# Kernel tuning notes

Hardware: AMD Instinct MI355X
Metric: run time of the kernel (lower is better)

Reference implementation:

```python
import jax, jax.numpy as jnp
import numpy as np

K = 3
STRIDE = 1
PAD = 1
DIL = 1


def setup_inputs() -> dict:
    key = jax.random.key(0)
    k1, k2, k3 = jax.random.split(key, 3)
    B, C, O, H, W = 8, 64, 64, 128, 128
    x = jax.random.normal(k1, (B, C, H, W), dtype=jnp.float32)
    # small offset-conv weights so predicted offsets stay in a sane range
    w_off = jax.random.normal(k2, (2 * K * K, C, K, K), dtype=jnp.float32) * 0.05
    b_off = jnp.zeros((2 * K * K,), dtype=jnp.float32)
    w_conv = jax.random.normal(k3, (O, C, K, K), dtype=jnp.float32) * (1.0 / np.sqrt(C * K * K))
    return {"x": x, "w_off": w_off, "b_off": b_off, "w_conv": w_conv}


def _offset_conv(x, w, b):
    y = jax.lax.conv_general_dilated(
        x, w, window_strides=(STRIDE, STRIDE),
        padding=[(PAD, PAD), (PAD, PAD)], rhs_dilation=(DIL, DIL),
        dimension_numbers=("NCHW", "OIHW", "NCHW"))
    return y + b[None, :, None, None]


def _deform_conv2d(x, offset, weight):
    # torchvision deform_conv2d v1, groups=1, offset_groups=1, no bias
    B, C, H, W = x.shape
    Ho, Wo = offset.shape[2], offset.shape[3]
    # offset channels laid out as (ky, kx, [dy, dx]) pairs
    off = offset.reshape(B, K, K, 2, Ho, Wo)
    dy, dx = off[:, :, :, 0], off[:, :, :, 1]           # [B,K,K,Ho,Wo]

    hs = (jnp.arange(Ho) * STRIDE - PAD).astype(offset.dtype)
    ws = (jnp.arange(Wo) * STRIDE - PAD).astype(offset.dtype)
    kk = (jnp.arange(K) * DIL).astype(offset.dtype)
    py = hs[None, None, None, :, None] + kk[None, :, None, None, None] + dy
    px = ws[None, None, None, None, :] + kk[None, None, :, None, None] + dx

    y0 = jnp.floor(py)
    x0 = jnp.floor(px)
    ly = py - y0
    lx = px - x0
    y0i = y0.astype(jnp.int32)
    x0i = x0.astype(jnp.int32)

    xf = x.reshape(B, C, H * W)

    def gather(yi, xi):
        valid = ((yi >= 0) & (yi < H) & (xi >= 0) & (xi < W)).astype(x.dtype)
        idx = jnp.clip(yi, 0, H - 1) * W + jnp.clip(xi, 0, W - 1)  # [B,K,K,Ho,Wo]
        idxf = idx.reshape(B, 1, -1)
        v = jnp.take_along_axis(xf, idxf, axis=2)                  # [B,C,K*K*Ho*Wo]
        v = v.reshape(B, C, K, K, Ho, Wo)
        return v * valid[:, None]                                  # zero-pad out of bounds

    ly_ = ly[:, None]  # broadcast over channel dim
    lx_ = lx[:, None]
    val = (gather(y0i, x0i) * (1 - ly_) * (1 - lx_)
           + gather(y0i, x0i + 1) * (1 - ly_) * lx_
           + gather(y0i + 1, x0i) * ly_ * (1 - lx_)
           + gather(y0i + 1, x0i + 1) * ly_ * lx_)   # [B,C,K,K,Ho,Wo]

    return jnp.einsum("bcklhw,ockl->bohw", val, weight)


def reference(x, w_off, b_off, w_conv):
    offset = _offset_conv(x, w_off, b_off)
    return _deform_conv2d(x, offset, w_conv)
```

## Files before the change

### kernel.cpp

```cpp
#include <hip/hip_runtime.h>

#define B_    8
#define C_    64
#define O_    64
#define H_    128
#define W_    128
#define HW_   (H_ * W_)
#define NOFF_ 18
#define KK_   9
#define TW_   19
#define PADW_ 5
#define RSTR_ 144

typedef __attribute__((ext_vector_type(8))) _Float16 f16x8;
typedef __attribute__((ext_vector_type(2))) _Float16 f16x2;
typedef __attribute__((ext_vector_type(4))) unsigned int u32x4;
typedef __attribute__((ext_vector_type(4))) float f32x4;
typedef unsigned int uint32;
typedef unsigned short ushort;

__device__ __forceinline__ f16x2 u2h(uint32 u) {
    union { uint32 u; f16x2 h; } c; c.u = u; return c.h;
}
__device__ __forceinline__ f16x8 u2h8(u32x4 q) {
    union { u32x4 u; f16x8 h; } c; c.u = q; return c.h;
}

#define GLOAD16(dst, a64) \
    asm volatile("global_load_dwordx4 %0, %1, off" : "=&v"(dst) : "v"(a64) : "memory")
#define WAITV_TIE(N, w) \
    asm volatile("s_waitcnt vmcnt(" #N ")" \
        : "+v"(w[0]), "+v"(w[1]), "+v"(w[2]), "+v"(w[3]), \
          "+v"(w[4]), "+v"(w[5]), "+v"(w[6]), "+v"(w[7]))
#define WAITV(N) do { \
    asm volatile("s_waitcnt vmcnt(" #N ")" ::: "memory"); \
    __builtin_amdgcn_sched_barrier(0); } while (0)
#define DRAIN_ALL() do { \
    asm volatile("s_waitcnt vmcnt(0) lgkmcnt(0)" ::: "memory"); \
    __builtin_amdgcn_sched_barrier(0); } while (0)

__global__ __launch_bounds__(256) void transpose_x(
    const float* __restrict__ x, _Float16* __restrict__ xT)
{
    __shared__ float tile[64][65];
    int blk = blockIdx.x;
    int b   = blk >> 8;
    int hw0 = (blk & 255) * 64;
    int t   = threadIdx.x;
    int q   = t >> 6;
    int ln  = t & 63;
#pragma unroll
    for (int p = 0; p < 16; ++p) {
        int c = p * 4 + q;
        tile[c][ln] = x[((size_t)(b * C_ + c) << 14) + hw0 + ln];
    }
    __syncthreads();
#pragma unroll
    for (int p = 0; p < 16; ++p) {
        int hw = p * 4 + q;
        xT[(((size_t)b << 14) + hw0 + hw) * 64 + ln] = (_Float16)tile[ln][hw];
    }
}

__global__ __launch_bounds__(256) void prep3(
    const float* __restrict__ w_conv, const float* __restrict__ w_off,
    _Float16* __restrict__ wfrag, _Float16* __restrict__ wofff)
{
    int idx = blockIdx.x * 256 + threadIdx.x;
    if (idx < 36864) {
        int i    = idx & 7;
        int lane = (idx >> 3) & 63;
        int nb   = (idx >> 9) & 3;
        int kc   = (idx >> 11) & 1;
        int kk   = idx >> 12;
        int c = kc * 32 + ((lane >> 4) << 3) + i;
        int o = nb * 16 + (lane & 15);
        wfrag[idx] = (_Float16)w_conv[(o * C_ + c) * 9 + kk];
    }
    if (idx < 18432) {
        int i    = idx & 7;
        int lane = (idx >> 3) & 63;
        int nb   = (idx >> 9) & 1;
        int kc   = (idx >> 10) & 1;
        int kk   = idx >> 11;
        int m = nb * 16 + (lane & 15);
        int c = kc * 32 + ((lane >> 4) << 3) + i;
        wofff[idx] = (_Float16)((m < NOFF_) ? w_off[(m * C_ + c) * 9 + kk] : 0.0f);
    }
}

__global__ __launch_bounds__(512, 2) void offconv_mfma5(
    const _Float16* __restrict__ xT, const _Float16* __restrict__ wofff,
    const float* __restrict__ b_off, _Float16* __restrict__ offsh)
{
    __shared__ _Float16 wlds[18432];
    int t = threadIdx.x;
    {
        const u32x4* src = (const u32x4*)wofff;
        u32x4* dst = (u32x4*)wlds;
#pragma unroll
        for (int r = 0; r < 5; ++r) {
            int i = r * 512 + t;
            if (i < 2304) dst[i] = src[i];
        }
    }
    DRAIN_ALL();
    __syncthreads();

    int blk  = blockIdx.x;
    int b    = blk & 7;
    int hw0  = (blk >> 3) * 128;
    int lane = t & 63;
    int wv   = t >> 6;
    int pxb  = hw0 + wv * 16;
    int pr   = lane & 15;
    int g    = lane >> 4;
    int px   = pxb + pr;
    int h = px >> 7, w = px & (W_ - 1);
    const _Float16* xb = xT + (((size_t)b << 14) << 6);

    f32x4 acc[2];
#pragma unroll
    for (int nb = 0; nb < 2; ++nb) acc[nb] = (f32x4){0.f, 0.f, 0.f, 0.f};

    u32x4 q[3][2];
    bool  vld[3];

    auto issueO = [&](int kk, int st) {
        int ky = kk / 3, kx = kk % 3;
        int yy = h - 1 + ky, xx = w - 1 + kx;
        vld[st] = ((unsigned)yy < (unsigned)H_) && ((unsigned)xx < (unsigned)W_);
        int src = (min(max(yy, 0), H_ - 1) << 7) + min(max(xx, 0), W_ - 1);
        unsigned long long a = (unsigned long long)(xb + ((size_t)src << 6) + g * 8);
        GLOAD16(q[st][0], a);
        unsigned long long a2 = a + 64;
        GLOAD16(q[st][1], a2);
    };

    issueO(0, 0); issueO(1, 1); issueO(2, 2);
#pragma unroll
    for (int kk = 0; kk < KK_; ++kk) {
        const int s = kk % 3;
        if (kk < 7)      { WAITV(4); }
        else if (kk < 8) { WAITV(2); }
        else             { WAITV(0); }
#pragma unroll
        for (int kc = 0; kc < 2; ++kc) {
            f16x8 a = u2h8(q[s][kc]);
            f16x8 z = {};
            a = vld[s] ? a : z;
#pragma unroll
            for (int nb = 0; nb < 2; ++nb) {
                f16x8 bfr = *(const f16x8*)(wlds +
                    ((((kk * 2 + kc) << 1) + nb) << 9) + (lane << 3));
                acc[nb] = __builtin_amdgcn_mfma_f32_16x16x32_f16(a, bfr, acc[nb], 0, 0, 0);
            }
        }
        if (kk < 6) issueO(kk + 3, s);
    }

#pragma unroll
    for (int nb = 0; nb < 2; ++nb) {
        int m = nb * 16 + pr;
        if (m < NOFF_) {
            float bias = b_off[m];
#pragma unroll
            for (int r = 0; r < 4; ++r) {
                int prow = pxb + g * 4 + r;
                offsh[(size_t)((b << 14) + prow) * NOFF_ + m] = (_Float16)(acc[nb][r] + bias);
            }
        }
    }
}

__global__ __launch_bounds__(256, 3) void deform_mfma10(
    const _Float16* __restrict__ xT, const _Float16* __restrict__ offsh,
    const _Float16* __restrict__ wfrag, float* __restrict__ out)
{
    __shared__ char tilec[TW_ * TW_ * RSTR_];

    int t    = threadIdx.x;
    int blk  = blockIdx.x;
    int b    = blk & 7;
    int tid  = blk >> 3;
    int ty   = tid >> 4, tx = tid & 15;
    int lane = t & 63;
    int wv   = t >> 6;
    int pr   = lane & 15;
    int gg   = lane >> 4;
    int ry0  = ty * 8 - PADW_;
    int cx0  = tx * 8 - PADW_;
    const _Float16* xb = xT + (((size_t)b << 14) << 6);

#pragma unroll
    for (int it = 0; it < 12; ++it) {
        int idx = it * 256 + t;
        if (idx < TW_ * TW_ * 8) {
            int i   = idx / (TW_ * 8);
            int rem = idx - i * (TW_ * 8);
            int j   = rem >> 3, cg = rem & 7;
            int yy = min(max(ry0 + i, 0), H_ - 1);
            int xx = min(max(cx0 + j, 0), W_ - 1);
            u32x4 v = *(const u32x4*)(xb + (((size_t)((yy << 7) + xx)) << 6) + (cg << 3));
            int rl = i * TW_ + j;
            *(u32x4*)(tilec + rl * RSTR_ + (cg << 4)) = v;
        }
    }

    int h_img = ty * 8 + wv * 2 + (pr >> 3);
    int w_img = tx * 8 + (pr & 7);
    const uint32* obu = (const uint32*)(offsh +
        (size_t)((b << 14) + (h_img << 7) + w_img) * NOFF_);
    uint32 dpk[9];
#pragma unroll
    for (int kk = 0; kk < 9; ++kk) dpk[kk] = obu[kk];
    DRAIN_ALL();
    __syncthreads();

    f32x4 acc[4];
#pragma unroll
    for (int nb = 0; nb < 4; ++nb) acc[nb] = (f32x4){0.f, 0.f, 0.f, 0.f};

    u32x4 wqA[8], wqB[8];
    u32x4 q[8];

    auto issueW = [&](int kk, u32x4* wq) {
#pragma unroll
        for (int f = 0; f < 8; ++f) {
            unsigned long long wa = (unsigned long long)(wfrag +
                ((((kk * 2 + (f >> 2)) << 2) + (f & 3)) << 9) + (lane << 3));
            GLOAD16(wq[f], wa);
        }
    };

    issueW(0, wqA);
#pragma unroll
    for (int kk = 0; kk < KK_; ++kk) {
        u32x4* wcur = (kk & 1) ? wqB : wqA;
        u32x4* wnxt = (kk & 1) ? wqA : wqB;
        if (kk < 8) issueW(kk + 1, wnxt);

        int ky = kk / 3, kx = kk % 3;
        union { uint32 u; f16x2 hh; } cv; cv.u = dpk[kk];
        float dyv = (float)cv.hh[0], dxv = (float)cv.hh[1];
        float py  = (float)(h_img - 1 + ky) + dyv;
        float pxf = (float)(w_img - 1 + kx) + dxv;
        float y0f = floorf(py), x0f = floorf(pxf);
        float ly = py - y0f, lx = pxf - x0f;
        int y0 = (int)y0f, x0 = (int)x0f;
        float w00 = (1.f - ly) * (1.f - lx);
        float w01 = (1.f - ly) * lx;
        float w10 = ly * (1.f - lx);
        float w11 = ly * lx;
        bool vy0 = (unsigned)y0       < (unsigned)H_;
        bool vy1 = (unsigned)(y0 + 1) < (unsigned)H_;
        bool vx0 = (unsigned)x0       < (unsigned)W_;
        bool vx1 = (unsigned)(x0 + 1) < (unsigned)W_;
        if (!(vy0 && vx0)) w00 = 0.f;
        if (!(vy0 && vx1)) w01 = 0.f;
        if (!(vy1 && vx0)) w10 = 0.f;
        if (!(vy1 && vx1)) w11 = 0.f;
        int yc0 = min(max(y0, 0), H_ - 1);
        int yc1 = min(max(y0 + 1, 0), H_ - 1);
        int xc0 = min(max(x0, 0), W_ - 1);
        int xc1 = min(max(x0 + 1, 0), W_ - 1);
        f16x2 Wc0 = (f16x2){(_Float16)w00, (_Float16)w00};
        f16x2 Wc1 = (f16x2){(_Float16)w01, (_Float16)w01};
        f16x2 Wc2 = (f16x2){(_Float16)w10, (_Float16)w10};
        f16x2 Wc3 = (f16x2){(_Float16)w11, (_Float16)w11};

        int r0 = yc0 - ry0, r1 = yc1 - ry0;
        int c0 = xc0 - cx0, c1 = xc1 - cx0;
        int bad = ((unsigned)r0 >= TW_) | ((unsigned)r1 >= TW_) |
                  ((unsigned)c0 >= TW_) | ((unsigned)c1 >= TW_);

        if (!__any(bad)) {
            int rl00 = r0 * TW_ + c0, rl01 = r0 * TW_ + c1;
            int rl10 = r1 * TW_ + c0, rl11 = r1 * TW_ + c1;
            int ch0 = gg << 4;
#pragma unroll
            for (int kc = 0; kc < 2; ++kc) {
                int ch = ch0 + (kc << 6);
                q[kc * 4 + 0] = *(const u32x4*)(tilec + rl00 * RSTR_ + ch);
                q[kc * 4 + 1] = *(const u32x4*)(tilec + rl01 * RSTR_ + ch);
                q[kc * 4 + 2] = *(const u32x4*)(tilec + rl10 * RSTR_ + ch);
                q[kc * 4 + 3] = *(const u32x4*)(tilec + rl11 * RSTR_ + ch);
            }
        } else {
#pragma unroll
            for (int kc = 0; kc < 2; ++kc) {
                int ce = ((kc << 2) + gg) << 3;
                unsigned long long a00 = (unsigned long long)(xb + (((size_t)((yc0 << 7) + xc0)) << 6) + ce);
                unsigned long long a01 = (unsigned long long)(xb + (((size_t)((yc0 << 7) + xc1)) << 6) + ce);
                unsigned long long a10 = (unsigned long long)(xb + (((size_t)((yc1 << 7) + xc0)) << 6) + ce);
                unsigned long long a11 = (unsigned long long)(xb + (((size_t)((yc1 << 7) + xc1)) << 6) + ce);
                GLOAD16(q[kc * 4 + 0], a00);
                GLOAD16(q[kc * 4 + 1], a01);
                GLOAD16(q[kc * 4 + 2], a10);
                GLOAD16(q[kc * 4 + 3], a11);
            }
            WAITV(0);
        }

        if (kk < 8) { WAITV_TIE(8, wcur); } else { WAITV_TIE(0, wcur); }

#pragma unroll
        for (int kc = 0; kc < 2; ++kc) {
            f16x8 a;
            f16x2* ap = (f16x2*)&a;
#pragma unroll
            for (int p4 = 0; p4 < 4; ++p4) {
                ap[p4] = u2h(q[kc * 4 + 0][p4]) * Wc0
                       + u2h(q[kc * 4 + 1][p4]) * Wc1
                       + u2h(q[kc * 4 + 2][p4]) * Wc2
                       + u2h(q[kc * 4 + 3][p4]) * Wc3;
            }
#pragma unroll
            for (int nb = 0; nb < 4; ++nb) {
                acc[nb] = __builtin_amdgcn_mfma_f32_16x16x32_f16(
                    a, u2h8(wcur[kc * 4 + nb]), acc[nb], 0, 0, 0);
            }
        }
    }

#pragma unroll
    for (int nb = 0; nb < 4; ++nb) {
        int o = nb * 16 + pr;
        int orow = ty * 8 + wv * 2 + (gg >> 1);
        int ocol = tx * 8 + ((gg & 1) << 2);
        float* outp = out + (((size_t)(b * O_ + o)) << 14) + (orow << 7) + ocol;
        *(f32x4*)outp = acc[nb];
    }
}

extern "C" void kernel_launch(void* const* d_in, const int* in_sizes, int n_in,
                              void* d_out, int out_size, void* d_ws, size_t ws_size,
                              hipStream_t stream)
{
    const float* x      = (const float*)d_in[0];
    const float* w_off  = (const float*)d_in[1];
    const float* b_off  = (const float*)d_in[2];
    const float* w_conv = (const float*)d_in[3];
    float* out = (float*)d_out;
    char* ws = (char*)d_ws;

    const size_t XT_OFF    = 0;
    const size_t OFFS_OFF  = 16777216;
    const size_t WFRAG_OFF = 21495808;
    const size_t WOFF_OFF  = 21569536;

    _Float16* xT    = (_Float16*)(ws + XT_OFF);
    _Float16* offsh = (_Float16*)(ws + OFFS_OFF);
    _Float16* wfrag = (_Float16*)(ws + WFRAG_OFF);
    _Float16* wofff = (_Float16*)(ws + WOFF_OFF);

    transpose_x  <<<2048, 256, 0, stream>>>(x, xT);
    prep3        <<<144, 256, 0, stream>>>(w_conv, w_off, wfrag, wofff);
    offconv_mfma5<<<1024, 512, 0, stream>>>(xT, wofff, b_off, offsh);
    deform_mfma10<<<2048, 256, 0, stream>>>(xT, offsh, wfrag, out);
}
```

Before: 65.63 us.

## Software-pipeline LDS sample reads across kernel taps and defer out-of-tile fixups

The deform kernel now prepares the bilinear coordinates and issues the LDS reads for tap kk+1 while computing the bilinear blend and MFMAs for tap kk, double-buffering the sample registers. Samples that fall outside the shared tile are first read from a clamped LDS position. They are then corrected in a separate pass afterwards, which reloads them from global memory and adds the difference through extra MFMAs. This removes the divergent branch and the full vmem drain from the main loop. The cost is more registers, so launch bounds drop to 2 waves per SIMD, plus extra work in the rare fixup path.

```diff
diff --git a/kernel.cpp b/kernel.cpp
--- a/kernel.cpp
+++ b/kernel.cpp
@@ -173,7 +173,7 @@
     }
 }
 
-__global__ __launch_bounds__(256, 3) void deform_mfma10(
+__global__ __launch_bounds__(256, 2) void deform_mfma12(
     const _Float16* __restrict__ xT, const _Float16* __restrict__ offsh,
     const _Float16* __restrict__ wfrag, float* __restrict__ out)
 {
@@ -221,25 +221,7 @@
 #pragma unroll
     for (int nb = 0; nb < 4; ++nb) acc[nb] = (f32x4){0.f, 0.f, 0.f, 0.f};
 
-    u32x4 wqA[8], wqB[8];
-    u32x4 q[8];
-
-    auto issueW = [&](int kk, u32x4* wq) {
-#pragma unroll
-        for (int f = 0; f < 8; ++f) {
-            unsigned long long wa = (unsigned long long)(wfrag +
-                ((((kk * 2 + (f >> 2)) << 2) + (f & 3)) << 9) + (lane << 3));
-            GLOAD16(wq[f], wa);
-        }
-    };
-
-    issueW(0, wqA);
-#pragma unroll
-    for (int kk = 0; kk < KK_; ++kk) {
-        u32x4* wcur = (kk & 1) ? wqB : wqA;
-        u32x4* wnxt = (kk & 1) ? wqA : wqB;
-        if (kk < 8) issueW(kk + 1, wnxt);
-
+    auto prepk = [&](int kk, f16x2* Wc, int* rlc, int* ycx) -> int {
         int ky = kk / 3, kx = kk % 3;
         union { uint32 u; f16x2 hh; } cv; cv.u = dpk[kk];
         float dyv = (float)cv.hh[0], dxv = (float)cv.hh[1];
@@ -264,61 +246,123 @@
         int yc1 = min(max(y0 + 1, 0), H_ - 1);
         int xc0 = min(max(x0, 0), W_ - 1);
         int xc1 = min(max(x0 + 1, 0), W_ - 1);
-        f16x2 Wc0 = (f16x2){(_Float16)w00, (_Float16)w00};
-        f16x2 Wc1 = (f16x2){(_Float16)w01, (_Float16)w01};
-        f16x2 Wc2 = (f16x2){(_Float16)w10, (_Float16)w10};
-        f16x2 Wc3 = (f16x2){(_Float16)w11, (_Float16)w11};
-
+        Wc[0] = (f16x2){(_Float16)w00, (_Float16)w00};
+        Wc[1] = (f16x2){(_Float16)w01, (_Float16)w01};
+        Wc[2] = (f16x2){(_Float16)w10, (_Float16)w10};
+        Wc[3] = (f16x2){(_Float16)w11, (_Float16)w11};
+        ycx[0] = yc0; ycx[1] = yc1; ycx[2] = xc0; ycx[3] = xc1;
         int r0 = yc0 - ry0, r1 = yc1 - ry0;
         int c0 = xc0 - cx0, c1 = xc1 - cx0;
         int bad = ((unsigned)r0 >= TW_) | ((unsigned)r1 >= TW_) |
                   ((unsigned)c0 >= TW_) | ((unsigned)c1 >= TW_);
-
-        if (!__any(bad)) {
-            int rl00 = r0 * TW_ + c0, rl01 = r0 * TW_ + c1;
-            int rl10 = r1 * TW_ + c0, rl11 = r1 * TW_ + c1;
-            int ch0 = gg << 4;
-#pragma unroll
-            for (int kc = 0; kc < 2; ++kc) {
-                int ch = ch0 + (kc << 6);
-                q[kc * 4 + 0] = *(const u32x4*)(tilec + rl00 * RSTR_ + ch);
-                q[kc * 4 + 1] = *(const u32x4*)(tilec + rl01 * RSTR_ + ch);
-                q[kc * 4 + 2] = *(const u32x4*)(tilec + rl10 * RSTR_ + ch);
-                q[kc * 4 + 3] = *(const u32x4*)(tilec + rl11 * RSTR_ + ch);
-            }
-        } else {
-#pragma unroll
-            for (int kc = 0; kc < 2; ++kc) {
-                int ce = ((kc << 2) + gg) << 3;
-                unsigned long long a00 = (unsigned long long)(xb + (((size_t)((yc0 << 7) + xc0)) << 6) + ce);
-                unsigned long long a01 = (unsigned long long)(xb + (((size_t)((yc0 << 7) + xc1)) << 6) + ce);
-                unsigned long long a10 = (unsigned long long)(xb + (((size_t)((yc1 << 7) + xc0)) << 6) + ce);
-                unsigned long long a11 = (unsigned long long)(xb + (((size_t)((yc1 << 7) + xc1)) << 6) + ce);
-                GLOAD16(q[kc * 4 + 0], a00);
-                GLOAD16(q[kc * 4 + 1], a01);
-                GLOAD16(q[kc * 4 + 2], a10);
-                GLOAD16(q[kc * 4 + 3], a11);
-            }
-            WAITV(0);
-        }
+        r0 = min(max(r0, 0), TW_ - 1); r1 = min(max(r1, 0), TW_ - 1);
+        c0 = min(max(c0, 0), TW_ - 1); c1 = min(max(c1, 0), TW_ - 1);
+        rlc[0] = r0 * TW_ + c0; rlc[1] = r0 * TW_ + c1;
+        rlc[2] = r1 * TW_ + c0; rlc[3] = r1 * TW_ + c1;
+        return bad;
+    };
+    auto ldsRead = [&](const int* rlc, u32x4* q) {
+#pragma unroll
+        for (int kc = 0; kc < 2; ++kc) {
+            int ch = (gg << 4) + (kc << 6);
+#pragma unroll
+            for (int cr = 0; cr < 4; ++cr)
+                q[kc * 4 + cr] = *(const u32x4*)(tilec + rlc[cr] * RSTR_ + ch);
+        }
+    };
+    auto issueW = [&](int kk, u32x4* wq) {
+#pragma unroll
+        for (int f = 0; f < 8; ++f) {
+            unsigned long long wa = (unsigned long long)(wfrag +
+                ((((kk * 2 + (f >> 2)) << 2) + (f & 3)) << 9) + (lane << 3));
+            GLOAD16(wq[f], wa);
+        }
+    };
+    auto bilerp = [&](const u32x4* q, const f16x2* Wc, int kc) -> f16x8 {
+        f16x8 a;
+        f16x2* ap = (f16x2*)&a;
+#pragma unroll
+        for (int p4 = 0; p4 < 4; ++p4) {
+            ap[p4] = u2h(q[kc * 4 + 0][p4]) * Wc[0]
+                   + u2h(q[kc * 4 + 1][p4]) * Wc[1]
+                   + u2h(q[kc * 4 + 2][p4]) * Wc[2]
+                   + u2h(q[kc * 4 + 3][p4]) * Wc[3];
+        }
+        return a;
+    };
+
+    u32x4 qA[8], qB[8], wqA[8], wqB[8];
+    f16x2 WcA[4], WcB[4];
+    int   rlA[4], rlB[4], ycxT[4];
+    uint32 badmask = 0;
+
+    issueW(0, wqA);
+    if (prepk(0, WcA, rlA, ycxT)) badmask |= 1u;
+    ldsRead(rlA, qA);
+
+#pragma unroll
+    for (int kk = 0; kk < KK_; ++kk) {
+        u32x4* wcur = (kk & 1) ? wqB : wqA;
+        u32x4* wnxt = (kk & 1) ? wqA : wqB;
+        u32x4* qcur = (kk & 1) ? qB : qA;
+        u32x4* qnxt = (kk & 1) ? qA : qB;
+        f16x2* Wcur = (kk & 1) ? WcB : WcA;
+        f16x2* Wnxt = (kk & 1) ? WcA : WcB;
+        int*   rlnx = (kk & 1) ? rlA : rlB;
+
+        if (kk < 8) {
+            issueW(kk + 1, wnxt);
+            if (prepk(kk + 1, Wnxt, rlnx, ycxT)) badmask |= (1u << (kk + 1));
+            ldsRead(rlnx, qnxt);
+        }
+
+        f16x8 a0 = bilerp(qcur, Wcur, 0);
+        f16x8 a1 = bilerp(qcur, Wcur, 1);
 
         if (kk < 8) { WAITV_TIE(8, wcur); } else { WAITV_TIE(0, wcur); }
 
 #pragma unroll
-        for (int kc = 0; kc < 2; ++kc) {
-            f16x8 a;
-            f16x2* ap = (f16x2*)&a;
-#pragma unroll
-            for (int p4 = 0; p4 < 4; ++p4) {
-                ap[p4] = u2h(q[kc * 4 + 0][p4]) * Wc0
-                       + u2h(q[kc * 4 + 1][p4]) * Wc1
-                       + u2h(q[kc * 4 + 2][p4]) * Wc2
-                       + u2h(q[kc * 4 + 3][p4]) * Wc3;
-            }
-#pragma unroll
-            for (int nb = 0; nb < 4; ++nb) {
-                acc[nb] = __builtin_amdgcn_mfma_f32_16x16x32_f16(
-                    a, u2h8(wcur[kc * 4 + nb]), acc[nb], 0, 0, 0);
+        for (int nb = 0; nb < 4; ++nb)
+            acc[nb] = __builtin_amdgcn_mfma_f32_16x16x32_f16(a0, u2h8(wcur[nb]), acc[nb], 0, 0, 0);
+#pragma unroll
+        for (int nb = 0; nb < 4; ++nb)
+            acc[nb] = __builtin_amdgcn_mfma_f32_16x16x32_f16(a1, u2h8(wcur[4 + nb]), acc[nb], 0, 0, 0);
+    }
+
+    if (__any((int)(badmask != 0))) {
+#pragma unroll 1
+        for (int kk = 0; kk < KK_; ++kk) {
+            int mybad = (badmask >> kk) & 1;
+            if (__any(mybad)) {
+                f16x2 Wc[4]; int rlc[4], ycx[4];
+                prepk(kk, Wc, rlc, ycx);
+                u32x4 qw[8], qr[8];
+                ldsRead(rlc, qw);
+#pragma unroll
+                for (int kc = 0; kc < 2; ++kc) {
+                    int ce = ((kc << 2) + gg) << 3;
+#pragma unroll
+                    for (int cr = 0; cr < 4; ++cr) {
+                        int yy = ycx[cr >> 1], xx = ycx[2 + (cr & 1)];
+                        unsigned long long a = (unsigned long long)(xb +
+                            (((size_t)((yy << 7) + xx)) << 6) + ce);
+                        GLOAD16(qr[kc * 4 + cr], a);
+                    }
+                }
+                issueW(kk, wqA);
+                WAITV(0);
+#pragma unroll
+                for (int kc = 0; kc < 2; ++kc) {
+                    f16x8 aw = bilerp(qw, Wc, kc);
+                    f16x8 ar = bilerp(qr, Wc, kc);
+                    f16x8 d  = ar - aw;
+                    f16x8 z  = {};
+                    d = mybad ? d : z;
+#pragma unroll
+                    for (int nb = 0; nb < 4; ++nb)
+                        acc[nb] = __builtin_amdgcn_mfma_f32_16x16x32_f16(
+                            d, u2h8(wqA[kc * 4 + nb]), acc[nb], 0, 0, 0);
+                }
             }
         }
     }
@@ -357,5 +401,5 @@
     transpose_x  <<<2048, 256, 0, stream>>>(x, xT);
     prep3        <<<144, 256, 0, stream>>>(w_conv, w_off, wfrag, wofff);
     offconv_mfma5<<<1024, 512, 0, stream>>>(xT, wofff, b_off, offsh);
-    deform_mfma10<<<2048, 256, 0, stream>>>(xT, offsh, wfrag, out);
-}
+    deform_mfma12<<<2048, 256, 0, stream>>>(xT, offsh, wfrag, out);
+}
```

Result: slower. 68.67 us (+4.6%).
